# Performance work log

Measured on AMD Instinct MI355X. Metric: run time of the kernel, lower is better.

The kernel has to match this reference:

```python
import jax, jax.numpy as jnp
import numpy as np

N, D, H, P, B = 6000, 256, 8, 128, 16
DH = D // H


def _layernorm(x, g, b, eps=1e-5):
    mu = jnp.mean(x, axis=-1, keepdims=True)
    var = jnp.mean((x - mu) ** 2, axis=-1, keepdims=True)
    return (x - mu) * jax.lax.rsqrt(var + eps) * g + b


def setup_inputs() -> dict:
    key = jax.random.key(0)
    ks = jax.random.split(key, 12)
    s = 1.0 / np.sqrt(D)
    inp = {
        "H_genes": jax.random.normal(ks[0], (N, D), jnp.float32),
        "perturbation_indices": jax.random.randint(ks[1], (P,), 0, N),
        "batch_assignment": jnp.sort(jax.random.randint(ks[2], (P,), 0, B)),
        "batch_size": B,
        # nn.MultiheadAttention params
        "in_proj_w": jax.random.uniform(ks[3], (3 * D, D), jnp.float32, -s, s),
        "in_proj_b": jnp.zeros((3 * D,), jnp.float32),
        "out_proj_w": jax.random.uniform(ks[4], (D, D), jnp.float32, -s, s),
        "out_proj_b": jnp.zeros((D,), jnp.float32),
        # FFN params
        "ffn_w1": jax.random.uniform(ks[5], (4 * D, D), jnp.float32, -s, s),
        "ffn_b1": jnp.zeros((4 * D,), jnp.float32),
        "ffn_w2": jax.random.uniform(ks[6], (D, 4 * D), jnp.float32, -1.0 / np.sqrt(4 * D), 1.0 / np.sqrt(4 * D)),
        "ffn_b2": jnp.zeros((D,), jnp.float32),
        # LayerNorms
        "ln1_g": jnp.ones((D,), jnp.float32),
        "ln1_b": jnp.zeros((D,), jnp.float32),
        "ln2_g": jnp.ones((D,), jnp.float32),
        "ln2_b": jnp.zeros((D,), jnp.float32),
    }
    return inp


def reference(H_genes, perturbation_indices, batch_assignment, batch_size,
              in_proj_w, in_proj_b, out_proj_w, out_proj_b,
              ffn_w1, ffn_b1, ffn_w2, ffn_b2,
              ln1_g, ln1_b, ln2_g, ln2_b):
    n, d = H_genes.shape
    Wq, Wk, Wv = jnp.split(in_proj_w, 3, axis=0)
    bq, bk, bv = jnp.split(in_proj_b, 3, axis=0)

    # queries: all genes (shared across batch); keys/values: ragged pert context
    q = (H_genes @ Wq.T + bq).reshape(n, H, DH)          # [N,h,dh]
    Hp = H_genes[perturbation_indices]                    # [P,d]
    k = (Hp @ Wk.T + bk).reshape(-1, H, DH)               # [P,h,dh]
    v = (Hp @ Wv.T + bv).reshape(-1, H, DH)               # [P,h,dh]

    scale = 1.0 / np.sqrt(DH)
    scores = jnp.einsum('nhe,phe->hnp', q * scale, k)     # shared scores [h,N,P]

    mask = batch_assignment[None, :] == jnp.arange(batch_size)[:, None]  # [B,P]
    logits = jnp.where(mask[:, None, None, :], scores[None], -1e9)       # [B,h,N,P]
    attn = jax.nn.softmax(logits, axis=-1)

    ctx = jnp.einsum('bhnp,phe->bnhe', attn, v).reshape(batch_size, n, d)
    attn_out = ctx @ out_proj_w.T + out_proj_b            # [B,N,d]

    # torch path: empty perturbation set -> zeros_like attention output
    has_any = mask.any(axis=-1).astype(attn_out.dtype)    # [B]
    attn_out = attn_out * has_any[:, None, None]

    x = _layernorm(H_genes[None] + attn_out, ln1_g, ln1_b)
    ffn = jax.nn.gelu(x @ ffn_w1.T + ffn_b1, approximate=False) @ ffn_w2.T + ffn_b2
    return _layernorm(x + ffn, ln2_g, ln2_b)
```

## Files before the change

kernel.cpp:

```cpp
#include <hip/hip_runtime.h>
#include <math.h>

#define N_GENES 6000
#define DM 256
#define NH 8
#define DHEAD 32
#define FF 1024
#define PMAX 128
#define MT 64
#define LDX 264

typedef unsigned short u16;
typedef unsigned int u32;
typedef __attribute__((ext_vector_type(8))) short s8bf;
typedef __attribute__((ext_vector_type(4))) float f4;

__device__ __forceinline__ f4 mfma_bf16(s8bf a, s8bf b, f4 c) {
    return __builtin_amdgcn_mfma_f32_16x16x32_bf16(a, b, c, 0, 0, 0);
}

__device__ __forceinline__ float bf2f(u16 u) { return __uint_as_float(((u32)u) << 16); }
__device__ __forceinline__ u16 f2bf(float f) {
    u32 x = __float_as_uint(f);
    return (u16)((x + 0x7fffu + ((x >> 16) & 1u)) >> 16);
}
__device__ __forceinline__ float gelu_exact(float x) {
    return 0.5f * x * (1.0f + erff(x * 0.70710678118654752f));
}

__global__ __launch_bounds__(256) void pack_kernel(const float* __restrict__ src,
                                                   u16* __restrict__ dst, int N, int K) {
    int c = blockIdx.x * 256 + threadIdx.x;
    int KT = K >> 5;
    int total = (N >> 4) * KT * 64;
    if (c >= total) return;
    int lane = c & 63;
    int k0i = (c >> 6) % KT;
    int nt = c / (KT << 6);
    const float* s = src + (size_t)(nt * 16 + (lane & 15)) * K + k0i * 32 + (lane >> 4) * 8;
    u16* d = dst + (size_t)c * 8;
    #pragma unroll
    for (int j = 0; j < 8; ++j) d[j] = f2bf(s[j]);
}

__global__ __launch_bounds__(256) void transpose_kernel(const float* __restrict__ src,
                                                        float* __restrict__ dst) {
    int i = blockIdx.x * 256 + threadIdx.x;
    int k = i >> 8, d = i & 255;
    dst[i] = src[(size_t)d * DM + k];
}

__global__ __launch_bounds__(256) void kvproj_kernel(
    const float* __restrict__ Hg, const int* __restrict__ pidx,
    const float* __restrict__ Win, const float* __restrict__ bin,
    float* __restrict__ kbuf, float* __restrict__ vbuf) {
    __shared__ float xs[DM];
    int p = blockIdx.x, d = threadIdx.x;
    int row = pidx[p];
    xs[d] = Hg[(size_t)row * DM + d];
    __syncthreads();
    const float4* wk = (const float4*)(Win + (size_t)(DM + d) * DM);
    const float4* wv = (const float4*)(Win + (size_t)(2 * DM + d) * DM);
    float ak = bin[DM + d];
    float av = bin[2 * DM + d];
    #pragma unroll 4
    for (int k = 0; k < DM / 4; ++k) {
        float4 a = wk[k], b = wv[k];
        float x0 = xs[4*k], x1 = xs[4*k+1], x2 = xs[4*k+2], x3 = xs[4*k+3];
        ak += a.x * x0 + a.y * x1 + a.z * x2 + a.w * x3;
        av += b.x * x0 + b.y * x1 + b.z * x2 + b.w * x3;
    }
    kbuf[(size_t)p * DM + d] = ak;
    vbuf[(size_t)p * DM + d] = av;
}

__global__ __launch_bounds__(512, 4) void fused_all_kernel(
    const float* __restrict__ Hg, const float* __restrict__ WqT,
    const float* __restrict__ bin,
    const float* __restrict__ kbuf, const float* __restrict__ vbuf,
    const int* __restrict__ assign,
    const u16* __restrict__ WoP, const float* __restrict__ bout,
    const u16* __restrict__ W1P, const float* __restrict__ b1p,
    const u16* __restrict__ W2P, const float* __restrict__ b2p,
    const float* __restrict__ g1, const float* __restrict__ bb1,
    const float* __restrict__ g2, const float* __restrict__ bb2,
    float* __restrict__ out, int P, int B) {

    __shared__ __align__(16) u16 xb[MT][LDX];
    __shared__ __align__(16) char reg2_raw[32 * 264 * 4];
    __shared__ int asg[PMAX];
    __shared__ int startb[16];
    __shared__ int cntb[16];
    __shared__ float hasb[16];

    float* reg2f = (float*)reg2_raw;
    float (*sc)[132] = (float(*)[132])reg2f;
    float* qs   = reg2f + 4224;
    float* hrow = reg2f + 5312;
    float* ps   = reg2f + 6336;
    float (*sb32)[264] = (float(*)[264])reg2_raw;
    u16  (*hb)[LDX]    = (u16 (*)[LDX])reg2_raw;

    const f4 fzero = {0.f, 0.f, 0.f, 0.f};
    int tid = threadIdx.x;
    int w = tid >> 6, l = tid & 63;
    int l15 = l & 15, q8 = (l >> 4) * 8, q4 = (l >> 4) * 4;
    int n0 = blockIdx.x * 4;

    if (tid < P) asg[tid] = assign[tid];
    for (int i = tid; i < 4 * DM; i += 512)
        hrow[i] = Hg[(size_t)n0 * DM + i];
    __syncthreads();
    if (tid < 16) {
        int s = 0, c = 0;
        for (int p = 0; p < P; ++p) { int a = asg[p]; s += (a < tid); c += (a == tid); }
        startb[tid] = s; cntb[tid] = c; hasb[tid] = c ? 1.f : 0.f;
    }

    {
        int d = tid & 255, kh = tid >> 8;
        const float* wt = WqT + (size_t)(kh * 128) * DM + d;
        float a0 = 0.f, a1 = 0.f, a2 = 0.f, a3 = 0.f;
        const float* h0 = hrow + kh * 128;
        #pragma unroll 8
        for (int k = 0; k < 128; ++k) {
            float wv = wt[(size_t)k * DM];
            a0 += wv * h0[k];
            a1 += wv * h0[256 + k];
            a2 += wv * h0[512 + k];
            a3 += wv * h0[768 + k];
        }
        ps[0 * 512 + kh * 256 + d] = a0;
        ps[1 * 512 + kh * 256 + d] = a1;
        ps[2 * 512 + kh * 256 + d] = a2;
        ps[3 * 512 + kh * 256 + d] = a3;
    }
    __syncthreads();
    for (int i = tid; i < 1024; i += 512) {
        int g = i >> 8, d = i & 255;
        float q = (ps[g * 512 + d] + ps[g * 512 + 256 + d] + bin[d]) * 0.17677669529663687f;
        qs[(g * 8 + (d >> 5)) * 34 + (d & 31)] = q;
    }
    __syncthreads();

    for (int idx = tid; idx < 32 * P; idx += 512) {
        int gh = idx & 31, p = idx >> 5;
        const float* qp = qs + gh * 34;
        const float4* kr = (const float4*)(kbuf + (size_t)p * DM + (gh & 7) * DHEAD);
        float dsum = 0.f;
        #pragma unroll
        for (int e = 0; e < 8; ++e) {
            float4 kv = kr[e];
            dsum += qp[4*e] * kv.x + qp[4*e+1] * kv.y + qp[4*e+2] * kv.z + qp[4*e+3] * kv.w;
        }
        sc[gh][p] = dsum;
    }
    __syncthreads();

    {
        int r = tid >> 3, h = tid & 7;
        int gi = r & 3, bb = r >> 2;
        int s = startb[bb], c = cntb[bb];
        float4 cx[8];
        #pragma unroll
        for (int e = 0; e < 8; ++e) cx[e] = make_float4(0.f, 0.f, 0.f, 0.f);
        if (c > 0) {
            const float* scp = sc[gi * 8 + h];
            float m = -INFINITY;
            for (int i = 0; i < c; ++i) m = fmaxf(m, scp[s + i]);
            float sum = 0.f;
            const float* vb0 = vbuf + h * DHEAD;
            for (int i = 0; i < c; ++i) {
                float wgt = __expf(scp[s + i] - m);
                sum += wgt;
                const float4* vr = (const float4*)(vb0 + (size_t)(s + i) * DM);
                #pragma unroll
                for (int e = 0; e < 8; ++e) {
                    float4 vvv = vr[e];
                    cx[e].x += wgt * vvv.x; cx[e].y += wgt * vvv.y;
                    cx[e].z += wgt * vvv.z; cx[e].w += wgt * vvv.w;
                }
            }
            float inv = 1.0f / sum;
            #pragma unroll
            for (int e = 0; e < 8; ++e) {
                cx[e].x *= inv; cx[e].y *= inv; cx[e].z *= inv; cx[e].w *= inv;
            }
        }
        u16* xrow = &xb[r][h * DHEAD];
        #pragma unroll
        for (int e = 0; e < 8; ++e) {
            *(u32*)(xrow + 4 * e)     = (u32)f2bf(cx[e].x) | ((u32)f2bf(cx[e].y) << 16);
            *(u32*)(xrow + 4 * e + 2) = (u32)f2bf(cx[e].z) | ((u32)f2bf(cx[e].w) << 16);
        }
    }
    __syncthreads();

    f4 acc[4][2] = {fzero, fzero, fzero, fzero, fzero, fzero, fzero, fzero};
    {
        const u16* pb0 = WoP + (size_t)w * 8192 + (size_t)l * 8;
        #pragma unroll 4
        for (int k0i = 0; k0i < 8; ++k0i) {
            int k0 = k0i * 32;
            s8bf a0 = *(const s8bf*)&xb[l15][k0 + q8];
            s8bf a1 = *(const s8bf*)&xb[16 + l15][k0 + q8];
            s8bf a2 = *(const s8bf*)&xb[32 + l15][k0 + q8];
            s8bf a3 = *(const s8bf*)&xb[48 + l15][k0 + q8];
            s8bf b0 = *(const s8bf*)(pb0 + k0i * 512);
            s8bf b1 = *(const s8bf*)(pb0 + 4096 + k0i * 512);
            acc[0][0] = mfma_bf16(a0, b0, acc[0][0]);
            acc[1][0] = mfma_bf16(a1, b0, acc[1][0]);
            acc[2][0] = mfma_bf16(a2, b0, acc[2][0]);
            acc[3][0] = mfma_bf16(a3, b0, acc[3][0]);
            acc[0][1] = mfma_bf16(a0, b1, acc[0][1]);
            acc[1][1] = mfma_bf16(a1, b1, acc[1][1]);
            acc[2][1] = mfma_bf16(a2, b1, acc[2][1]);
            acc[3][1] = mfma_bf16(a3, b1, acc[3][1]);
        }
    }

    auto ln1_pass = [&](int hf, f4 aA0, f4 aA1, f4 aB0, f4 aB1) {
        int cl = w * 32 + l15;
        #pragma unroll
        for (int r = 0; r < 4; ++r) {
            sb32[q4 + r][cl]           = aA0[r];
            sb32[q4 + r][cl + 16]      = aA1[r];
            sb32[16 + q4 + r][cl]      = aB0[r];
            sb32[16 + q4 + r][cl + 16] = aB1[r];
        }
        __syncthreads();
        int r32 = tid >> 4, c4 = (tid & 15) * 4;
        int row = hf * 32 + r32;
        int gi = row & 3, bb = row >> 2;
        float has = hasb[bb];
        const float* hp = Hg + (size_t)(n0 + gi) * DM;
        float tv[16];
        float sum = 0.f;
        #pragma unroll
        for (int jg = 0; jg < 4; ++jg) {
            int c = c4 + jg * 64;
            float4 hv = *(const float4*)(hp + c);
            float4 bv = *(const float4*)(bout + c);
            float t0 = hv.x + has * (sb32[r32][c]     + bv.x);
            float t1 = hv.y + has * (sb32[r32][c + 1] + bv.y);
            float t2 = hv.z + has * (sb32[r32][c + 2] + bv.z);
            float t3 = hv.w + has * (sb32[r32][c + 3] + bv.w);
            tv[jg*4] = t0; tv[jg*4+1] = t1; tv[jg*4+2] = t2; tv[jg*4+3] = t3;
            sum += t0 + t1 + t2 + t3;
        }
        sum += __shfl_xor(sum, 1, 16); sum += __shfl_xor(sum, 2, 16);
        sum += __shfl_xor(sum, 4, 16); sum += __shfl_xor(sum, 8, 16);
        float mu = sum * (1.0f / DM);
        float vs = 0.f;
        #pragma unroll
        for (int j = 0; j < 16; ++j) { float dd = tv[j] - mu; vs += dd * dd; }
        vs += __shfl_xor(vs, 1, 16); vs += __shfl_xor(vs, 2, 16);
        vs += __shfl_xor(vs, 4, 16); vs += __shfl_xor(vs, 8, 16);
        float rs = rsqrtf(vs * (1.0f / DM) + 1e-5f);
        #pragma unroll
        for (int jg = 0; jg < 4; ++jg) {
            int c = c4 + jg * 64;
            float x0 = (tv[jg*4]     - mu) * rs * g1[c]     + bb1[c];
            float x1 = (tv[jg*4 + 1] - mu) * rs * g1[c + 1] + bb1[c + 1];
            float x2 = (tv[jg*4 + 2] - mu) * rs * g1[c + 2] + bb1[c + 2];
            float x3 = (tv[jg*4 + 3] - mu) * rs * g1[c + 3] + bb1[c + 3];
            *(u32*)&xb[row][c]     = (u32)f2bf(x0) | ((u32)f2bf(x1) << 16);
            *(u32*)&xb[row][c + 2] = (u32)f2bf(x2) | ((u32)f2bf(x3) << 16);
        }
        __syncthreads();
    };
    ln1_pass(0, acc[0][0], acc[0][1], acc[1][0], acc[1][1]);
    ln1_pass(1, acc[2][0], acc[2][1], acc[3][0], acc[3][1]);

    f4 acc2[4][2] = {fzero, fzero, fzero, fzero, fzero, fzero, fzero, fzero};
    for (int ch = 0; ch < 4; ++ch) {
        f4 acc1[4][2] = {fzero, fzero, fzero, fzero, fzero, fzero, fzero, fzero};
        {
            const u16* pb0 = W1P + (size_t)(ch * 16 + 2 * w) * 4096 + (size_t)l * 8;
            #pragma unroll 4
            for (int k0i = 0; k0i < 8; ++k0i) {
                int k0 = k0i * 32;
                s8bf a0 = *(const s8bf*)&xb[l15][k0 + q8];
                s8bf a1 = *(const s8bf*)&xb[16 + l15][k0 + q8];
                s8bf a2 = *(const s8bf*)&xb[32 + l15][k0 + q8];
                s8bf a3 = *(const s8bf*)&xb[48 + l15][k0 + q8];
                s8bf b0 = *(const s8bf*)(pb0 + k0i * 512);
                s8bf b1 = *(const s8bf*)(pb0 + 4096 + k0i * 512);
                acc1[0][0] = mfma_bf16(a0, b0, acc1[0][0]);
                acc1[1][0] = mfma_bf16(a1, b0, acc1[1][0]);
                acc1[2][0] = mfma_bf16(a2, b0, acc1[2][0]);
                acc1[3][0] = mfma_bf16(a3, b0, acc1[3][0]);
                acc1[0][1] = mfma_bf16(a0, b1, acc1[0][1]);
                acc1[1][1] = mfma_bf16(a1, b1, acc1[1][1]);
                acc1[2][1] = mfma_bf16(a2, b1, acc1[2][1]);
                acc1[3][1] = mfma_bf16(a3, b1, acc1[3][1]);
            }
        }
        {
            int cl = w * 32 + l15;
            float bbA = b1p[ch * 256 + cl];
            float bbB = b1p[ch * 256 + cl + 16];
            #pragma unroll
            for (int mt = 0; mt < 4; ++mt)
                #pragma unroll
                for (int r = 0; r < 4; ++r) {
                    hb[mt * 16 + q4 + r][cl]      = f2bf(gelu_exact(acc1[mt][0][r] + bbA));
                    hb[mt * 16 + q4 + r][cl + 16] = f2bf(gelu_exact(acc1[mt][1][r] + bbB));
                }
        }
        __syncthreads();
        {
            const u16* pb0 = W2P + (size_t)(2 * w) * 16384 + (size_t)(ch * 8) * 512 + (size_t)l * 8;
            #pragma unroll 4
            for (int k0i = 0; k0i < 8; ++k0i) {
                int k0 = k0i * 32;
                s8bf a0 = *(const s8bf*)&hb[l15][k0 + q8];
                s8bf a1 = *(const s8bf*)&hb[16 + l15][k0 + q8];
                s8bf a2 = *(const s8bf*)&hb[32 + l15][k0 + q8];
                s8bf a3 = *(const s8bf*)&hb[48 + l15][k0 + q8];
                s8bf b0 = *(const s8bf*)(pb0 + k0i * 512);
                s8bf b1 = *(const s8bf*)(pb0 + 16384 + k0i * 512);
                acc2[0][0] = mfma_bf16(a0, b0, acc2[0][0]);
                acc2[1][0] = mfma_bf16(a1, b0, acc2[1][0]);
                acc2[2][0] = mfma_bf16(a2, b0, acc2[2][0]);
                acc2[3][0] = mfma_bf16(a3, b0, acc2[3][0]);
                acc2[0][1] = mfma_bf16(a0, b1, acc2[0][1]);
                acc2[1][1] = mfma_bf16(a1, b1, acc2[1][1]);
                acc2[2][1] = mfma_bf16(a2, b1, acc2[2][1]);
                acc2[3][1] = mfma_bf16(a3, b1, acc2[3][1]);
            }
        }
        __syncthreads();
    }

    auto ln2_pass = [&](int hf, f4 aA0, f4 aA1, f4 aB0, f4 aB1) {
        int cl = w * 32 + l15;
        #pragma unroll
        for (int r = 0; r < 4; ++r) {
            sb32[q4 + r][cl]           = aA0[r];
            sb32[q4 + r][cl + 16]      = aA1[r];
            sb32[16 + q4 + r][cl]      = aB0[r];
            sb32[16 + q4 + r][cl + 16] = aB1[r];
        }
        __syncthreads();
        int r32 = tid >> 4, c4 = (tid & 15) * 4;
        int row = hf * 32 + r32;
        int gi = row & 3, bb = row >> 2;
        float tv[16];
        float sum = 0.f;
        #pragma unroll
        for (int jg = 0; jg < 4; ++jg) {
            int c = c4 + jg * 64;
            float4 bv = *(const float4*)(b2p + c);
            float t0 = bf2f(xb[row][c])     + sb32[r32][c]     + bv.x;
            float t1 = bf2f(xb[row][c + 1]) + sb32[r32][c + 1] + bv.y;
            float t2 = bf2f(xb[row][c + 2]) + sb32[r32][c + 2] + bv.z;
            float t3 = bf2f(xb[row][c + 3]) + sb32[r32][c + 3] + bv.w;
            tv[jg*4] = t0; tv[jg*4+1] = t1; tv[jg*4+2] = t2; tv[jg*4+3] = t3;
            sum += t0 + t1 + t2 + t3;
        }
        sum += __shfl_xor(sum, 1, 16); sum += __shfl_xor(sum, 2, 16);
        sum += __shfl_xor(sum, 4, 16); sum += __shfl_xor(sum, 8, 16);
        float mu = sum * (1.0f / DM);
        float vs = 0.f;
        #pragma unroll
        for (int j = 0; j < 16; ++j) { float dd = tv[j] - mu; vs += dd * dd; }
        vs += __shfl_xor(vs, 1, 16); vs += __shfl_xor(vs, 2, 16);
        vs += __shfl_xor(vs, 4, 16); vs += __shfl_xor(vs, 8, 16);
        float rs = rsqrtf(vs * (1.0f / DM) + 1e-5f);
        size_t gr = (size_t)bb * N_GENES + (size_t)(n0 + gi);
        float* op = out + gr * DM;
        #pragma unroll
        for (int jg = 0; jg < 4; ++jg) {
            int c = c4 + jg * 64;
            float4 y;
            y.x = (tv[jg*4]     - mu) * rs * g2[c]     + bb2[c];
            y.y = (tv[jg*4 + 1] - mu) * rs * g2[c + 1] + bb2[c + 1];
            y.z = (tv[jg*4 + 2] - mu) * rs * g2[c + 2] + bb2[c + 2];
            y.w = (tv[jg*4 + 3] - mu) * rs * g2[c + 3] + bb2[c + 3];
            *(float4*)(op + c) = y;
        }
        __syncthreads();
    };
    ln2_pass(0, acc2[0][0], acc2[0][1], acc2[1][0], acc2[1][1]);
    ln2_pass(1, acc2[2][0], acc2[2][1], acc2[3][0], acc2[3][1]);
}

__global__ __launch_bounds__(256) void attn_fb_kernel(
    const float* __restrict__ Hg, const float* __restrict__ kbuf, const float* __restrict__ vbuf,
    const int* __restrict__ assign, const float* __restrict__ Win, const float* __restrict__ bin,
    const float* __restrict__ Wout, const float* __restrict__ bout,
    const float* __restrict__ ln1g, const float* __restrict__ ln1b,
    float* __restrict__ xout, int P) {
    __shared__ float qs[DM];
    __shared__ float hrow[DM];
    __shared__ float sc[NH][PMAX + 1];
    __shared__ float ctxs[DM];
    __shared__ int asg[PMAX];
    __shared__ float red[4];

    int n = blockIdx.x, b = blockIdx.y, tid = threadIdx.x;
    if (tid < P) asg[tid] = assign[tid];
    hrow[tid] = Hg[(size_t)n * DM + tid];
    __syncthreads();
    {
        const float4* wr = (const float4*)(Win + (size_t)tid * DM);
        float acc = bin[tid];
        #pragma unroll 4
        for (int k = 0; k < DM / 4; ++k) {
            float4 w = wr[k];
            acc += w.x * hrow[4*k] + w.y * hrow[4*k+1] + w.z * hrow[4*k+2] + w.w * hrow[4*k+3];
        }
        qs[tid] = acc * 0.17677669529663687f;
        __syncthreads();
    }
    int start = 0, cnt = 0;
    for (int p = 0; p < P; ++p) { int a = asg[p]; start += (a < b); cnt += (a == b); }
    for (int idx = tid; idx < NH * cnt; idx += 256) {
        int h = idx & (NH - 1), pl = idx >> 3;
        const float* krow = kbuf + (size_t)(start + pl) * DM + h * DHEAD;
        const float* qh = qs + h * DHEAD;
        float acc = 0.f;
        #pragma unroll
        for (int e = 0; e < DHEAD; ++e) acc += qh[e] * krow[e];
        sc[h][pl] = acc;
    }
    __syncthreads();
    if (cnt > 0) {
        int h = tid >> 5, ll = tid & 31;
        float m = -INFINITY;
        for (int p = ll; p < cnt; p += 32) m = fmaxf(m, sc[h][p]);
        #pragma unroll
        for (int off = 16; off > 0; off >>= 1) m = fmaxf(m, __shfl_xor(m, off, 32));
        float s = 0.f;
        for (int p = ll; p < cnt; p += 32) { float e = __expf(sc[h][p] - m); sc[h][p] = e; s += e; }
        #pragma unroll
        for (int off = 16; off > 0; off >>= 1) s += __shfl_xor(s, off, 32);
        float inv = 1.0f / s;
        for (int p = ll; p < cnt; p += 32) sc[h][p] *= inv;
    }
    __syncthreads();
    {
        int hh = tid >> 5, e = tid & 31;
        float acc = 0.f;
        for (int p = 0; p < cnt; ++p)
            acc += sc[hh][p] * vbuf[(size_t)(start + p) * DM + hh * DHEAD + e];
        ctxs[tid] = acc;
    }
    __syncthreads();
    float ao = 0.f;
    if (cnt > 0) {
        ao = bout[tid];
        const float4* wr = (const float4*)(Wout + (size_t)tid * DM);
        #pragma unroll 4
        for (int k = 0; k < DM / 4; ++k) {
            float4 w = wr[k];
            ao += w.x * ctxs[4*k] + w.y * ctxs[4*k+1] + w.z * ctxs[4*k+2] + w.w * ctxs[4*k+3];
        }
    }
    float t = hrow[tid] + ao;
    {
        float v = t;
        #pragma unroll
        for (int off = 32; off > 0; off >>= 1) v += __shfl_down(v, off, 64);
        if ((tid & 63) == 0) red[tid >> 6] = v;
        __syncthreads();
        float mu = (red[0] + red[1] + red[2] + red[3]) * (1.0f / DM);
        __syncthreads();
        float dv = t - mu, v2 = dv * dv;
        #pragma unroll
        for (int off = 32; off > 0; off >>= 1) v2 += __shfl_down(v2, off, 64);
        if ((tid & 63) == 0) red[tid >> 6] = v2;
        __syncthreads();
        float var = (red[0] + red[1] + red[2] + red[3]) * (1.0f / DM);
        float xv = dv * rsqrtf(var + 1e-5f) * ln1g[tid] + ln1b[tid];
        xout[((size_t)b * N_GENES + n) * DM + tid] = xv;
    }
}

__global__ __launch_bounds__(256) void ffn_fb_kernel(
    float* __restrict__ xio, const float* __restrict__ W1, const float* __restrict__ b1,
    const float* __restrict__ W2, const float* __restrict__ b2,
    const float* __restrict__ ln2g, const float* __restrict__ ln2b) {
    __shared__ float xs[4][DM];
    __shared__ float hs[4][FF];
    __shared__ float red[4];
    int tid = threadIdx.x;
    size_t row0 = (size_t)blockIdx.x * 4;
    for (int i = tid; i < 4 * DM; i += 256)
        ((float*)xs)[i] = xio[row0 * DM + i];
    __syncthreads();
    for (int oi = 0; oi < FF / 256; ++oi) {
        int o = oi * 256 + tid;
        float bb = b1[o];
        float a0 = bb, a1 = bb, a2 = bb, a3 = bb;
        const float4* wr = (const float4*)(W1 + (size_t)o * DM);
        #pragma unroll 2
        for (int k = 0; k < DM / 4; ++k) {
            float4 w = wr[k];
            a0 += w.x * xs[0][4*k] + w.y * xs[0][4*k+1] + w.z * xs[0][4*k+2] + w.w * xs[0][4*k+3];
            a1 += w.x * xs[1][4*k] + w.y * xs[1][4*k+1] + w.z * xs[1][4*k+2] + w.w * xs[1][4*k+3];
            a2 += w.x * xs[2][4*k] + w.y * xs[2][4*k+1] + w.z * xs[2][4*k+2] + w.w * xs[2][4*k+3];
            a3 += w.x * xs[3][4*k] + w.y * xs[3][4*k+1] + w.z * xs[3][4*k+2] + w.w * xs[3][4*k+3];
        }
        hs[0][o] = gelu_exact(a0); hs[1][o] = gelu_exact(a1);
        hs[2][o] = gelu_exact(a2); hs[3][o] = gelu_exact(a3);
    }
    __syncthreads();
    int d = tid;
    float bb2 = b2[d];
    float c0 = bb2, c1 = bb2, c2 = bb2, c3 = bb2;
    const float4* wr = (const float4*)(W2 + (size_t)d * FF);
    #pragma unroll 2
    for (int k = 0; k < FF / 4; ++k) {
        float4 w = wr[k];
        c0 += w.x * hs[0][4*k] + w.y * hs[0][4*k+1] + w.z * hs[0][4*k+2] + w.w * hs[0][4*k+3];
        c1 += w.x * hs[1][4*k] + w.y * hs[1][4*k+1] + w.z * hs[1][4*k+2] + w.w * hs[1][4*k+3];
        c2 += w.x * hs[2][4*k] + w.y * hs[2][4*k+1] + w.z * hs[2][4*k+2] + w.w * hs[2][4*k+3];
        c3 += w.x * hs[3][4*k] + w.y * hs[3][4*k+1] + w.z * hs[3][4*k+2] + w.w * hs[3][4*k+3];
    }
    float cr[4] = {c0, c1, c2, c3};
    float g = ln2g[d], bln = ln2b[d];
    #pragma unroll
    for (int r = 0; r < 4; ++r) {
        float t = cr[r] + xs[r][d];
        float v = t;
        #pragma unroll
        for (int off = 32; off > 0; off >>= 1) v += __shfl_down(v, off, 64);
        if ((tid & 63) == 0) red[tid >> 6] = v;
        __syncthreads();
        float mu = (red[0] + red[1] + red[2] + red[3]) * (1.0f / DM);
        __syncthreads();
        float dv = t - mu, v2 = dv * dv;
        #pragma unroll
        for (int off = 32; off > 0; off >>= 1) v2 += __shfl_down(v2, off, 64);
        if ((tid & 63) == 0) red[tid >> 6] = v2;
        __syncthreads();
        float var = (red[0] + red[1] + red[2] + red[3]) * (1.0f / DM);
        float y = dv * rsqrtf(var + 1e-5f) * g + bln;
        xio[(row0 + r) * DM + d] = y;
        __syncthreads();
    }
}

extern "C" void kernel_launch(void* const* d_in, const int* in_sizes, int n_in,
                              void* d_out, int out_size, void* d_ws, size_t ws_size,
                              hipStream_t stream) {
    const float* Hg   = (const float*)d_in[0];
    const int* pidx   = (const int*)d_in[1];
    const int* assign = (const int*)d_in[2];
    const float* in_w = (const float*)d_in[4];
    const float* in_b = (const float*)d_in[5];
    const float* out_w= (const float*)d_in[6];
    const float* out_b= (const float*)d_in[7];
    const float* w1   = (const float*)d_in[8];
    const float* b1   = (const float*)d_in[9];
    const float* w2   = (const float*)d_in[10];
    const float* b2   = (const float*)d_in[11];
    const float* g1   = (const float*)d_in[12];
    const float* bb1  = (const float*)d_in[13];
    const float* g2   = (const float*)d_in[14];
    const float* bb2  = (const float*)d_in[15];

    int P = in_sizes[1];
    int B = out_size / (N_GENES * DM);
    size_t nrows = (size_t)B * N_GENES;
    float* out = (float*)d_out;

    size_t woB = (size_t)DM * DM;
    size_t w1B = (size_t)FF * DM;
    size_t w2B = (size_t)DM * FF;
    size_t wqTf = (size_t)DM * DM;
    size_t wbytes = (woB + w1B + w2B) * sizeof(u16) + wqTf * sizeof(float);
    size_t kvbytes = 2 * (size_t)P * DM * sizeof(float);

    if (ws_size >= wbytes + kvbytes && P <= PMAX && B == 16 && (N_GENES % 4) == 0) {
        u16* WoP  = (u16*)d_ws;
        u16* W1P  = WoP + woB;
        u16* W2P  = W1P + w1B;
        float* WqT = (float*)(W2P + w2B);
        float* kbuf = WqT + wqTf;
        float* vbuf = kbuf + (size_t)P * DM;

        pack_kernel<<<32, 256, 0, stream>>>(out_w, WoP, DM, DM);
        pack_kernel<<<128, 256, 0, stream>>>(w1, W1P, FF, DM);
        pack_kernel<<<128, 256, 0, stream>>>(w2, W2P, DM, FF);
        transpose_kernel<<<256, 256, 0, stream>>>(in_w, WqT);
        kvproj_kernel<<<P, 256, 0, stream>>>(Hg, pidx, in_w, in_b, kbuf, vbuf);
        fused_all_kernel<<<N_GENES / 4, 512, 0, stream>>>(
            Hg, WqT, in_b, kbuf, vbuf, assign,
            WoP, out_b, W1P, b1, W2P, b2, g1, bb1, g2, bb2, out, P, B);
    } else {
        float* kbuf = (float*)d_ws;
        float* vbuf = kbuf + (size_t)P * DM;
        kvproj_kernel<<<P, 256, 0, stream>>>(Hg, pidx, in_w, in_b, kbuf, vbuf);
        attn_fb_kernel<<<dim3(N_GENES, B), 256, 0, stream>>>(
            Hg, kbuf, vbuf, assign, in_w, in_b, out_w, out_b, g1, bb1, out, P);
        ffn_fb_kernel<<<(unsigned)(nrows / 4), 256, 0, stream>>>(
            out, w1, b1, w2, b2, g2, bb2);
    }
}
```

Before: 492.8 us.

## Merge prep kernels, prefetch MFMA operands, use fast GELU approximation

Combines the three weight-pack launches, the transpose and the K/V projection into a single prep kernel with block-range dispatch, and the transpose now goes through a shared-memory tile. In the out-proj, FFN1 and FFN2 MFMA loops the next k-step's weight fragments are loaded one iteration ahead, and the loops are fully unrolled. The exact erf GELU is replaced by an Abramowitz-Stegun polynomial with __expf. The fp32 staging stride changes to 260 to cut LDS bank conflicts. Together these aim to reduce launch overhead, load latency and GELU cost, at the price of a small GELU approximation error and higher register pressure.

```diff
diff --git a/kernel.cpp b/kernel.cpp
--- a/kernel.cpp
+++ b/kernel.cpp
@@ -9,6 +9,7 @@
 #define PMAX 128
 #define MT 64
 #define LDX 264
+#define LDF 260
 
 typedef unsigned short u16;
 typedef unsigned int u32;
@@ -27,27 +28,76 @@
 __device__ __forceinline__ float gelu_exact(float x) {
     return 0.5f * x * (1.0f + erff(x * 0.70710678118654752f));
 }
-
-__global__ __launch_bounds__(256) void pack_kernel(const float* __restrict__ src,
-                                                   u16* __restrict__ dst, int N, int K) {
-    int c = blockIdx.x * 256 + threadIdx.x;
-    int KT = K >> 5;
-    int total = (N >> 4) * KT * 64;
-    if (c >= total) return;
-    int lane = c & 63;
-    int k0i = (c >> 6) % KT;
-    int nt = c / (KT << 6);
-    const float* s = src + (size_t)(nt * 16 + (lane & 15)) * K + k0i * 32 + (lane >> 4) * 8;
-    u16* d = dst + (size_t)c * 8;
-    #pragma unroll
-    for (int j = 0; j < 8; ++j) d[j] = f2bf(s[j]);
-}
-
-__global__ __launch_bounds__(256) void transpose_kernel(const float* __restrict__ src,
-                                                        float* __restrict__ dst) {
-    int i = blockIdx.x * 256 + threadIdx.x;
-    int k = i >> 8, d = i & 255;
-    dst[i] = src[(size_t)d * DM + k];
+__device__ __forceinline__ float gelu_fast(float x) {
+    float z = fabsf(x) * 0.70710678118654752f;
+    float t = 1.0f / (1.0f + 0.3275911f * z);
+    float poly = t * (0.254829592f + t * (-0.284496736f + t * (1.421413741f +
+                 t * (-1.453152027f + t * 1.061405429f))));
+    float erf_abs = 1.0f - poly * __expf(-z * z);
+    float erfv = copysignf(erf_abs, x);
+    return 0.5f * x * (1.0f + erfv);
+}
+
+__global__ __launch_bounds__(256) void prep_kernel(
+    const float* __restrict__ Hg, const int* __restrict__ pidx,
+    const float* __restrict__ in_w, const float* __restrict__ in_b,
+    const float* __restrict__ out_w, const float* __restrict__ w1,
+    const float* __restrict__ w2,
+    u16* __restrict__ WoP, u16* __restrict__ W1P, u16* __restrict__ W2P,
+    float* __restrict__ WqT, float* __restrict__ kbuf, float* __restrict__ vbuf,
+    int P) {
+    __shared__ float ts[32][33];
+    __shared__ float xs[DM];
+    int blk = blockIdx.x, tid = threadIdx.x;
+    if (blk < 288) {
+        const float* src; u16* dst; int K; int c;
+        if (blk < 32)       { src = out_w; dst = WoP; K = DM; c = blk * 256 + tid; }
+        else if (blk < 160) { src = w1;    dst = W1P; K = DM; c = (blk - 32) * 256 + tid; }
+        else                { src = w2;    dst = W2P; K = FF; c = (blk - 160) * 256 + tid; }
+        int KT = K >> 5;
+        int lane = c & 63;
+        int k0i = (c >> 6) % KT;
+        int nt = c / (KT << 6);
+        const float* s = src + (size_t)(nt * 16 + (lane & 15)) * K + k0i * 32 + (lane >> 4) * 8;
+        u16* d = dst + (size_t)c * 8;
+        #pragma unroll
+        for (int j = 0; j < 8; ++j) d[j] = f2bf(s[j]);
+    } else if (blk < 352) {
+        int tile = blk - 288;
+        int tr = tile >> 3, tc = tile & 7;
+        int lane = tid & 31, rowg = tid >> 5;
+        #pragma unroll
+        for (int i = 0; i < 4; ++i) {
+            int r = rowg * 4 + i;
+            ts[r][lane] = in_w[(size_t)(tr * 32 + r) * DM + tc * 32 + lane];
+        }
+        __syncthreads();
+        #pragma unroll
+        for (int i = 0; i < 4; ++i) {
+            int a = rowg * 4 + i;
+            WqT[(size_t)(tc * 32 + a) * DM + tr * 32 + lane] = ts[lane][a];
+        }
+    } else {
+        int p = blk - 352;
+        if (p >= P) return;
+        int d = tid;
+        int row = pidx[p];
+        xs[d] = Hg[(size_t)row * DM + d];
+        __syncthreads();
+        const float4* wk = (const float4*)(in_w + (size_t)(DM + d) * DM);
+        const float4* wv = (const float4*)(in_w + (size_t)(2 * DM + d) * DM);
+        float ak = in_b[DM + d];
+        float av = in_b[2 * DM + d];
+        #pragma unroll 4
+        for (int k = 0; k < DM / 4; ++k) {
+            float4 a = wk[k], b = wv[k];
+            float x0 = xs[4*k], x1 = xs[4*k+1], x2 = xs[4*k+2], x3 = xs[4*k+3];
+            ak += a.x * x0 + a.y * x1 + a.z * x2 + a.w * x3;
+            av += b.x * x0 + b.y * x1 + b.z * x2 + b.w * x3;
+        }
+        kbuf[(size_t)p * DM + d] = ak;
+        vbuf[(size_t)p * DM + d] = av;
+    }
 }
 
 __global__ __launch_bounds__(256) void kvproj_kernel(
@@ -87,7 +137,7 @@
     float* __restrict__ out, int P, int B) {
 
     __shared__ __align__(16) u16 xb[MT][LDX];
-    __shared__ __align__(16) char reg2_raw[32 * 264 * 4];
+    __shared__ __align__(16) char reg2_raw[MT * LDX * 2];
     __shared__ int asg[PMAX];
     __shared__ int startb[16];
     __shared__ int cntb[16];
@@ -98,7 +148,7 @@
     float* qs   = reg2f + 4224;
     float* hrow = reg2f + 5312;
     float* ps   = reg2f + 6336;
-    float (*sb32)[264] = (float(*)[264])reg2_raw;
+    float (*sb32)[LDF] = (float(*)[LDF])reg2_raw;
     u16  (*hb)[LDX]    = (u16 (*)[LDX])reg2_raw;
 
     const f4 fzero = {0.f, 0.f, 0.f, 0.f};
@@ -198,16 +248,25 @@
 
     f4 acc[4][2] = {fzero, fzero, fzero, fzero, fzero, fzero, fzero, fzero};
     {
-        const u16* pb0 = WoP + (size_t)w * 8192 + (size_t)l * 8;
-        #pragma unroll 4
+        const u16* pb = WoP + (size_t)w * 8192 + (size_t)l * 8;
+        s8bf b0 = *(const s8bf*)(pb);
+        s8bf b1 = *(const s8bf*)(pb + 4096);
+        s8bf a0 = *(const s8bf*)&xb[l15][q8];
+        s8bf a1 = *(const s8bf*)&xb[16 + l15][q8];
+        s8bf a2 = *(const s8bf*)&xb[32 + l15][q8];
+        s8bf a3 = *(const s8bf*)&xb[48 + l15][q8];
+        #pragma unroll
         for (int k0i = 0; k0i < 8; ++k0i) {
-            int k0 = k0i * 32;
-            s8bf a0 = *(const s8bf*)&xb[l15][k0 + q8];
-            s8bf a1 = *(const s8bf*)&xb[16 + l15][k0 + q8];
-            s8bf a2 = *(const s8bf*)&xb[32 + l15][k0 + q8];
-            s8bf a3 = *(const s8bf*)&xb[48 + l15][k0 + q8];
-            s8bf b0 = *(const s8bf*)(pb0 + k0i * 512);
-            s8bf b1 = *(const s8bf*)(pb0 + 4096 + k0i * 512);
+            s8bf nb0, nb1, na0, na1, na2, na3;
+            if (k0i < 7) {
+                nb0 = *(const s8bf*)(pb + (k0i + 1) * 512);
+                nb1 = *(const s8bf*)(pb + 4096 + (k0i + 1) * 512);
+                int k0 = (k0i + 1) * 32 + q8;
+                na0 = *(const s8bf*)&xb[l15][k0];
+                na1 = *(const s8bf*)&xb[16 + l15][k0];
+                na2 = *(const s8bf*)&xb[32 + l15][k0];
+                na3 = *(const s8bf*)&xb[48 + l15][k0];
+            }
             acc[0][0] = mfma_bf16(a0, b0, acc[0][0]);
             acc[1][0] = mfma_bf16(a1, b0, acc[1][0]);
             acc[2][0] = mfma_bf16(a2, b0, acc[2][0]);
@@ -216,6 +275,7 @@
             acc[1][1] = mfma_bf16(a1, b1, acc[1][1]);
             acc[2][1] = mfma_bf16(a2, b1, acc[2][1]);
             acc[3][1] = mfma_bf16(a3, b1, acc[3][1]);
+            if (k0i < 7) { b0 = nb0; b1 = nb1; a0 = na0; a1 = na1; a2 = na2; a3 = na3; }
         }
     }
 
@@ -276,16 +336,21 @@
     for (int ch = 0; ch < 4; ++ch) {
         f4 acc1[4][2] = {fzero, fzero, fzero, fzero, fzero, fzero, fzero, fzero};
         {
-            const u16* pb0 = W1P + (size_t)(ch * 16 + 2 * w) * 4096 + (size_t)l * 8;
-            #pragma unroll 4
+            const u16* pb = W1P + (size_t)(ch * 16 + 2 * w) * 4096 + (size_t)l * 8;
+            s8bf b0 = *(const s8bf*)(pb);
+            s8bf b1 = *(const s8bf*)(pb + 4096);
+            #pragma unroll
             for (int k0i = 0; k0i < 8; ++k0i) {
-                int k0 = k0i * 32;
-                s8bf a0 = *(const s8bf*)&xb[l15][k0 + q8];
-                s8bf a1 = *(const s8bf*)&xb[16 + l15][k0 + q8];
-                s8bf a2 = *(const s8bf*)&xb[32 + l15][k0 + q8];
-                s8bf a3 = *(const s8bf*)&xb[48 + l15][k0 + q8];
-                s8bf b0 = *(const s8bf*)(pb0 + k0i * 512);
-                s8bf b1 = *(const s8bf*)(pb0 + 4096 + k0i * 512);
+                s8bf nb0, nb1;
+                if (k0i < 7) {
+                    nb0 = *(const s8bf*)(pb + (k0i + 1) * 512);
+                    nb1 = *(const s8bf*)(pb + 4096 + (k0i + 1) * 512);
+                }
+                int k0 = k0i * 32 + q8;
+                s8bf a0 = *(const s8bf*)&xb[l15][k0];
+                s8bf a1 = *(const s8bf*)&xb[16 + l15][k0];
+                s8bf a2 = *(const s8bf*)&xb[32 + l15][k0];
+                s8bf a3 = *(const s8bf*)&xb[48 + l15][k0];
                 acc1[0][0] = mfma_bf16(a0, b0, acc1[0][0]);
                 acc1[1][0] = mfma_bf16(a1, b0, acc1[1][0]);
                 acc1[2][0] = mfma_bf16(a2, b0, acc1[2][0]);
@@ -294,6 +359,7 @@
                 acc1[1][1] = mfma_bf16(a1, b1, acc1[1][1]);
                 acc1[2][1] = mfma_bf16(a2, b1, acc1[2][1]);
                 acc1[3][1] = mfma_bf16(a3, b1, acc1[3][1]);
+                if (k0i < 7) { b0 = nb0; b1 = nb1; }
             }
         }
         {
@@ -304,22 +370,27 @@
             for (int mt = 0; mt < 4; ++mt)
                 #pragma unroll
                 for (int r = 0; r < 4; ++r) {
-                    hb[mt * 16 + q4 + r][cl]      = f2bf(gelu_exact(acc1[mt][0][r] + bbA));
-                    hb[mt * 16 + q4 + r][cl + 16] = f2bf(gelu_exact(acc1[mt][1][r] + bbB));
+                    hb[mt * 16 + q4 + r][cl]      = f2bf(gelu_fast(acc1[mt][0][r] + bbA));
+                    hb[mt * 16 + q4 + r][cl + 16] = f2bf(gelu_fast(acc1[mt][1][r] + bbB));
                 }
         }
         __syncthreads();
         {
-            const u16* pb0 = W2P + (size_t)(2 * w) * 16384 + (size_t)(ch * 8) * 512 + (size_t)l * 8;
-            #pragma unroll 4
+            const u16* pb = W2P + (size_t)(2 * w) * 16384 + (size_t)(ch * 8) * 512 + (size_t)l * 8;
+            s8bf b0 = *(const s8bf*)(pb);
+            s8bf b1 = *(const s8bf*)(pb + 16384);
+            #pragma unroll
             for (int k0i = 0; k0i < 8; ++k0i) {
-                int k0 = k0i * 32;
-                s8bf a0 = *(const s8bf*)&hb[l15][k0 + q8];
-                s8bf a1 = *(const s8bf*)&hb[16 + l15][k0 + q8];
-                s8bf a2 = *(const s8bf*)&hb[32 + l15][k0 + q8];
-                s8bf a3 = *(const s8bf*)&hb[48 + l15][k0 + q8];
-                s8bf b0 = *(const s8bf*)(pb0 + k0i * 512);
-                s8bf b1 = *(const s8bf*)(pb0 + 16384 + k0i * 512);
+                s8bf nb0, nb1;
+                if (k0i < 7) {
+                    nb0 = *(const s8bf*)(pb + (k0i + 1) * 512);
+                    nb1 = *(const s8bf*)(pb + 16384 + (k0i + 1) * 512);
+                }
+                int k0 = k0i * 32 + q8;
+                s8bf a0 = *(const s8bf*)&hb[l15][k0];
+                s8bf a1 = *(const s8bf*)&hb[16 + l15][k0];
+                s8bf a2 = *(const s8bf*)&hb[32 + l15][k0];
+                s8bf a3 = *(const s8bf*)&hb[48 + l15][k0];
                 acc2[0][0] = mfma_bf16(a0, b0, acc2[0][0]);
                 acc2[1][0] = mfma_bf16(a1, b0, acc2[1][0]);
                 acc2[2][0] = mfma_bf16(a2, b0, acc2[2][0]);
@@ -328,6 +399,7 @@
                 acc2[1][1] = mfma_bf16(a1, b1, acc2[1][1]);
                 acc2[2][1] = mfma_bf16(a2, b1, acc2[2][1]);
                 acc2[3][1] = mfma_bf16(a3, b1, acc2[3][1]);
+                if (k0i < 7) { b0 = nb0; b1 = nb1; }
             }
         }
         __syncthreads();
@@ -582,11 +654,9 @@
         float* kbuf = WqT + wqTf;
         float* vbuf = kbuf + (size_t)P * DM;
 
-        pack_kernel<<<32, 256, 0, stream>>>(out_w, WoP, DM, DM);
-        pack_kernel<<<128, 256, 0, stream>>>(w1, W1P, FF, DM);
-        pack_kernel<<<128, 256, 0, stream>>>(w2, W2P, DM, FF);
-        transpose_kernel<<<256, 256, 0, stream>>>(in_w, WqT);
-        kvproj_kernel<<<P, 256, 0, stream>>>(Hg, pidx, in_w, in_b, kbuf, vbuf);
+        prep_kernel<<<352 + P, 256, 0, stream>>>(
+            Hg, pidx, in_w, in_b, out_w, w1, w2,
+            WoP, W1P, W2P, WqT, kbuf, vbuf, P);
         fused_all_kernel<<<N_GENES / 4, 512, 0, stream>>>(
             Hg, WqT, in_b, kbuf, vbuf, assign,
             WoP, out_b, W1P, b1, W2P, b2, g1, bb1, g2, bb2, out, P, B);
```

Result: no change. 484.3 us (-1.7%).
